# Kernel tuning notes

Measured on AMD Instinct MI355X. Metric: run time of the kernel, lower is better.

## Reference

```python
import jax, jax.numpy as jnp
import numpy as np

B, H, D = 4096, 200, 64
HID = 64


def setup_inputs() -> dict:
    key = jax.random.key(0)
    ks = jax.random.split(key, 12)
    s = 1.0 / np.sqrt(HID)
    return {
        "x": jax.random.normal(ks[0], (B, H, D), jnp.float32),
        "pos_query": jax.random.normal(ks[1], (B, D), jnp.float32),
        "lengths": jax.random.randint(ks[2], (B,), 1, H + 1, jnp.int32),
        "W_ih": jax.random.normal(ks[3], (3 * HID, D), jnp.float32) * s,
        "W_hh": jax.random.normal(ks[4], (3 * HID, HID), jnp.float32) * s,
        "b_ih": jax.random.normal(ks[5], (3 * HID,), jnp.float32) * s,
        "b_hh": jax.random.normal(ks[6], (3 * HID,), jnp.float32) * s,
        "aW_ih": jax.random.normal(ks[7], (3 * HID, HID), jnp.float32) * s,
        "aW_hh": jax.random.normal(ks[8], (3 * HID, HID), jnp.float32) * s,
        "ab_ih": jax.random.normal(ks[9], (3 * HID,), jnp.float32) * s,
        "ab_hh": jax.random.normal(ks[10], (3 * HID,), jnp.float32) * s,
    }


def _gates(x_t, h, W_i, W_h, b_i, b_h):
    gi = x_t @ W_i.T + b_i  # (B, 3H), PyTorch gate order [r, z, n]
    gh = h @ W_h.T + b_h
    gir, giz, gin = jnp.split(gi, 3, axis=-1)
    ghr, ghz, ghn = jnp.split(gh, 3, axis=-1)
    r = jax.nn.sigmoid(gir + ghr)
    z = jax.nn.sigmoid(giz + ghz)
    n = jnp.tanh(gin + r * ghn)
    return z, n


def _forward(x, pos_query, lengths, W_ih, W_hh, b_ih, b_hh, aW_ih, aW_hh, ab_ih, ab_hh):
    # mask[t, b] = True for valid (packed) timesteps
    mask = (jnp.arange(H)[:, None] < lengths[None, :])[:, :, None]  # (H, B, 1)
    xt = jnp.swapaxes(x, 0, 1)  # (H, B, D) time-major

    # --- GRU over packed sequence; padded positions output 0 (pad_packed_sequence) ---
    def gru_step(h, inp):
        x_t, m = inp
        z, n = _gates(x_t, h, W_ih, W_hh, b_ih, b_hh)
        h_new = (1.0 - z) * n + z * h
        h = jnp.where(m, h_new, h)
        return h, jnp.where(m, h_new, 0.0)

    h0 = jnp.zeros((x.shape[0], HID), x.dtype)
    _, out = jax.lax.scan(gru_step, h0, (xt, mask))  # out: (H, B, HID)

    # --- attention over full H (padded scores are 0, matching the torch code) ---
    scores = jnp.einsum("bd,hbd->bh", pos_query, out)  # (B, H)
    att = jax.nn.softmax(scores, axis=1)  # (B, H)

    # --- AUGRU: update gate scaled by attention score, masked to valid steps ---
    att_t = att.T[:, :, None]  # (H, B, 1)

    def augru_step(h, inp):
        o_t, a_t, m = inp
        u, n = _gates(o_t, h, aW_ih, aW_hh, ab_ih, ab_hh)
        u = a_t * u
        h_new = (1.0 - u) * h + u * n
        h = jnp.where(m, h_new, h)
        return h, None

    h_last, _ = jax.lax.scan(augru_step, h0, (out, att_t, mask))
    # h frozen past each sequence's length -> h_last == state at t = length-1
    return h_last  # (B, HID)


def reference(x, pos_query, lengths, W_ih, W_hh, b_ih, b_hh, aW_ih, aW_hh, ab_ih, ab_hh):
    return _forward(x, pos_query, lengths, W_ih, W_hh, b_ih, b_hh,
                    aW_ih, aW_hh, ab_ih, ab_hh)
```

## Files before the change

kernel.cpp:

```cpp
#include <hip/hip_runtime.h>
#include <hip/hip_bf16.h>


#define Bq   4096
#define Tq   200
#define BT   16

typedef __attribute__((ext_vector_type(8))) short short8;
typedef __attribute__((ext_vector_type(4))) float f32x4;

#define MFMA(a, b, c) __builtin_amdgcn_mfma_f32_16x16x32_bf16((a), (b), (c), 0, 0, 0)

#define LGKM_BARRIER()                                      \
  do {                                                      \
    __builtin_amdgcn_sched_barrier(0);                      \
    asm volatile("s_waitcnt lgkmcnt(0)" ::: "memory");      \
    __builtin_amdgcn_s_barrier();                           \
    asm volatile("" ::: "memory");                          \
    __builtin_amdgcn_sched_barrier(0);                      \
  } while (0)

static __device__ __forceinline__ int swz(int row, int colshort) {
  return row * 64 + ((((colshort) << 1) ^ ((row & 7) << 4)) >> 1);
}

static __device__ __forceinline__ unsigned pk2(float a, float b) {
  __hip_bfloat162 t = __float22bfloat162_rn(make_float2(a, b));
  unsigned r;
  __builtin_memcpy(&r, &t, sizeof(r));
  return r;
}
static __device__ __forceinline__ void pack4(f32x4 v, uint2 &H, uint2 &L) {
  H.x = pk2(v[0], v[1]);
  H.y = pk2(v[2], v[3]);
  float l0 = v[0] - __uint_as_float(H.x << 16);
  float l1 = v[1] - __uint_as_float(H.x & 0xffff0000u);
  float l2 = v[2] - __uint_as_float(H.y << 16);
  float l3 = v[3] - __uint_as_float(H.y & 0xffff0000u);
  L.x = pk2(l0, l1);
  L.y = pk2(l2, l3);
}
static __device__ __forceinline__ float sigm(float x) {
  return __builtin_amdgcn_rcpf(1.0f + __expf(-x));
}
static __device__ __forceinline__ float tanh_(float x) {
  return 2.0f * __builtin_amdgcn_rcpf(1.0f + __expf(-2.0f * x)) - 1.0f;
}
static __device__ __forceinline__ void split8(f32x4 a, f32x4 b, short8 &hi, short8 &lo) {
  uint2 H, L;
  pack4(a, H, L);
  hi[0] = (short)(H.x & 0xffff); hi[1] = (short)(H.x >> 16);
  hi[2] = (short)(H.y & 0xffff); hi[3] = (short)(H.y >> 16);
  lo[0] = (short)(L.x & 0xffff); lo[1] = (short)(L.x >> 16);
  lo[2] = (short)(L.y & 0xffff); lo[3] = (short)(L.y >> 16);
  pack4(b, H, L);
  hi[4] = (short)(H.x & 0xffff); hi[5] = (short)(H.x >> 16);
  hi[6] = (short)(H.y & 0xffff); hi[7] = (short)(H.y >> 16);
  lo[4] = (short)(L.x & 0xffff); lo[5] = (short)(L.x >> 16);
  lo[6] = (short)(L.y & 0xffff); lo[7] = (short)(L.y >> 16);
}

#define GI_X18(dR, dZ, dN, XH, XL)                   \
  _Pragma("unroll")                                  \
  for (int kc = 0; kc < 2; ++kc) {                   \
    dR = MFMA(wiH[0][kc], XH[kc], dR);               \
    dR = MFMA(wiH[0][kc], XL[kc], dR);               \
    dR = MFMA(wiL[0][kc], XH[kc], dR);               \
    dZ = MFMA(wiH[1][kc], XH[kc], dZ);               \
    dZ = MFMA(wiH[1][kc], XL[kc], dZ);               \
    dZ = MFMA(wiL[1][kc], XH[kc], dZ);               \
    dN = MFMA(wiH[2][kc], XH[kc], dN);               \
    dN = MFMA(wiH[2][kc], XL[kc], dN);               \
    dN = MFMA(wiL[2][kc], XH[kc], dN);               \
  }

#define GI_X12(dR, dZ, dN, XB)                       \
  _Pragma("unroll")                                  \
  for (int kc = 0; kc < 2; ++kc) {                   \
    dR = MFMA(wiH[0][kc], XB[kc], dR);               \
    dR = MFMA(wiL[0][kc], XB[kc], dR);               \
    dZ = MFMA(wiH[1][kc], XB[kc], dZ);               \
    dZ = MFMA(wiL[1][kc], XB[kc], dZ);               \
    dN = MFMA(wiH[2][kc], XB[kc], dN);               \
    dN = MFMA(wiL[2][kc], XB[kc], dN);               \
  }

#define GH18(dR, dZ, dNh)                            \
  _Pragma("unroll")                                  \
  for (int kc = 0; kc < 2; ++kc) {                   \
    dR  = MFMA(whH[0][kc], hH[kc], dR);              \
    dR  = MFMA(whH[0][kc], hL[kc], dR);              \
    dR  = MFMA(whL[0][kc], hH[kc], dR);              \
    dZ  = MFMA(whH[1][kc], hH[kc], dZ);              \
    dZ  = MFMA(whH[1][kc], hL[kc], dZ);              \
    dZ  = MFMA(whL[1][kc], hH[kc], dZ);              \
    dNh = MFMA(whH[2][kc], hH[kc], dNh);             \
    dNh = MFMA(whH[2][kc], hL[kc], dNh);             \
    dNh = MFMA(whL[2][kc], hH[kc], dNh);             \
  }

#define LOAD_WEIGHTS(WI, WH)                                                  \
  _Pragma("unroll")                                                           \
  for (int gt = 0; gt < 3; ++gt)                                              \
  _Pragma("unroll")                                                           \
    for (int kc = 0; kc < 2; ++kc) {                                          \
      const float* p = WI + (size_t)(gt * 64 + jh + c) * 64 + kc * 32 + g * 8;\
      split8(*(const f32x4*)p, *(const f32x4*)(p + 4), wiH[gt][kc], wiL[gt][kc]); \
      const float* q = WH + (size_t)(gt * 64 + jh + c) * 64 + kc * 32 + g * 8;\
      split8(*(const f32x4*)q, *(const f32x4*)(q + 4), whH[gt][kc], whL[gt][kc]); \
    }

#define LOAD_BIASES(BI, BH)                                                   \
  {                                                                           \
    f32x4 bi0 = *(const f32x4*)(BI + 0 * 64 + jh + 4 * g);                    \
    f32x4 bh0 = *(const f32x4*)(BH + 0 * 64 + jh + 4 * g);                    \
    f32x4 bi1 = *(const f32x4*)(BI + 1 * 64 + jh + 4 * g);                    \
    f32x4 bh1 = *(const f32x4*)(BH + 1 * 64 + jh + 4 * g);                    \
    bR = bi0 + bh0; bZ = bi1 + bh1;                                           \
    bNi = *(const f32x4*)(BI + 2 * 64 + jh + 4 * g);                          \
    bNh = *(const f32x4*)(BH + 2 * 64 + jh + 4 * g);                          \
  }

__global__ __launch_bounds__(256, 1)
void gru_fwd(const float* __restrict__ x, const float* __restrict__ pq,
             const int* __restrict__ lengths,
             const float* __restrict__ Wih, const float* __restrict__ Whh,
             const float* __restrict__ bih, const float* __restrict__ bhh,
             unsigned short* __restrict__ outbf,
             float* __restrict__ scores)
{
  __shared__ alignas(16) unsigned short hbH[2][1024], hbL[2][1024];
  __shared__ alignas(16) unsigned short xbH[2][1024], xbL[2][1024];
  __shared__ float slds[2][4][16];

  const int tid  = threadIdx.x;
  const int w    = tid >> 6;
  const int lane = tid & 63;
  const int c    = lane & 15;
  const int g    = lane >> 4;
  const int jh   = w * 16;
  const int b_g  = blockIdx.x * BT + c;

  const int pb   = tid >> 4;
  const int pd   = 4 * (tid & 15);
  const int pb_g = blockIdx.x * BT + pb;

  for (int i = tid; i < 1024; i += 256) { hbH[0][i] = 0; hbL[0][i] = 0; }

#pragma unroll
  for (int t0 = 0; t0 < 2; ++t0) {
    f32x4 xf = *(const f32x4*)(x + (size_t)pb_g * Tq * 64 + t0 * 64 + pd);
    uint2 H, L; pack4(xf, H, L);
    const int si = swz(pb, pd);
    *(uint2*)&xbH[t0][si] = H;
    *(uint2*)&xbL[t0][si] = L;
  }

  short8 wiH[3][2], wiL[3][2], whH[3][2], whL[3][2];
  LOAD_WEIGHTS(Wih, Whh);
  f32x4 bR, bZ, bNi, bNh;
  LOAD_BIASES(bih, bhh);
  const f32x4 pqv = *(const f32x4*)(pq + (size_t)b_g * 64 + jh + 4 * g);
  const int len = lengths[b_g];

  __syncthreads();

  f32x4 giR = bR, giZ = bZ, giN = bNi;
  {
    short8 xH[2], xL[2];
#pragma unroll
    for (int kc = 0; kc < 2; ++kc) {
      const int si = swz(c, kc * 32 + g * 8);
      xH[kc] = *(const short8*)&xbH[0][si];
      xL[kc] = *(const short8*)&xbL[0][si];
    }
    GI_X18(giR, giZ, giN, xH, xL);
  }

  f32x4 hreg = {0.f, 0.f, 0.f, 0.f};

  for (int t = 0; t < Tq; ++t) {
    const int cur = t & 1, nxt = cur ^ 1;
    const bool more = (t + 1 < Tq);

    f32x4 xf = {0.f, 0.f, 0.f, 0.f};
    if (t + 2 < Tq)
      xf = *(const f32x4*)(x + (size_t)pb_g * Tq * 64 + (size_t)(t + 2) * 64 + pd);

    short8 hH[2], hL[2], xnH[2], xnL[2];
#pragma unroll
    for (int kc = 0; kc < 2; ++kc) {
      const int si = swz(c, kc * 32 + g * 8);
      hH[kc] = *(const short8*)&hbH[cur][si];
      hL[kc] = *(const short8*)&hbL[cur][si];
    }
    if (more) {
#pragma unroll
      for (int kc = 0; kc < 2; ++kc) {
        const int si = swz(c, kc * 32 + g * 8);
        xnH[kc] = *(const short8*)&xbH[nxt][si];
        xnL[kc] = *(const short8*)&xbL[nxt][si];
      }
    }

    if (t > 0 && w == 0 && lane < 16) {
      float s = slds[nxt][0][lane] + slds[nxt][1][lane] +
                slds[nxt][2][lane] + slds[nxt][3][lane];
      scores[(size_t)(blockIdx.x * BT + lane) * Tq + (t - 1)] = s;
    }

    f32x4 aNh = bNh;
    GH18(giR, giZ, aNh);

    const bool valid = t < len;
    f32x4 outv;
#pragma unroll
    for (int r = 0; r < 4; ++r) {
      float rr = sigm(giR[r]);
      float zz = sigm(giZ[r]);
      float nn = tanh_(giN[r] + rr * aNh[r]);
      float hn = (1.f - zz) * nn + zz * hreg[r];
      hreg[r] = valid ? hn : hreg[r];
      outv[r] = valid ? hn : 0.f;
    }

    {
      uint2 H, L;
      pack4(hreg, H, L);
      const int si = swz(c, jh + 4 * g);
      *(uint2*)&hbH[nxt][si] = H;
      *(uint2*)&hbL[nxt][si] = L;
    }

    float sp = outv[0] * pqv[0] + outv[1] * pqv[1] + outv[2] * pqv[2] + outv[3] * pqv[3];
    sp += __shfl_xor(sp, 16);
    sp += __shfl_xor(sp, 32);
    if (lane < 16) slds[cur][w][lane] = sp;

    {
      uint2 O;
      O.x = pk2(outv[0], outv[1]);
      O.y = pk2(outv[2], outv[3]);
      *(uint2*)(outbf + (size_t)t * Bq * 64 + (size_t)b_g * 64 + jh + 4 * g) = O;
    }

    f32x4 nR = bR, nZ = bZ, nN = bNi;
    if (more) { GI_X18(nR, nZ, nN, xnH, xnL); }

    if (t + 2 < Tq) {
      uint2 H, L; pack4(xf, H, L);
      const int si = swz(pb, pd);
      *(uint2*)&xbH[cur][si] = H;
      *(uint2*)&xbL[cur][si] = L;
    }

    LGKM_BARRIER();
    giR = nR; giZ = nZ; giN = nN;
  }

  if (w == 0 && lane < 16) {
    const int pb2 = (Tq - 1) & 1;
    float s = slds[pb2][0][lane] + slds[pb2][1][lane] +
              slds[pb2][2][lane] + slds[pb2][3][lane];
    scores[(size_t)(blockIdx.x * BT + lane) * Tq + (Tq - 1)] = s;
  }
}

__global__ __launch_bounds__(256)
void softmax_att(const float* __restrict__ scores, float* __restrict__ att)
{
  const int w = threadIdx.x >> 6, lane = threadIdx.x & 63;
  const int row = blockIdx.x * 4 + w;
  const float* s = scores + (size_t)row * Tq;
  float v0 = s[lane], v1 = s[lane + 64], v2 = s[lane + 128];
  float v3 = (lane < Tq - 192) ? s[lane + 192] : -1e30f;
  float m = fmaxf(fmaxf(v0, v1), fmaxf(v2, v3));
#pragma unroll
  for (int off = 32; off >= 1; off >>= 1) m = fmaxf(m, __shfl_xor(m, off));
  float e0 = __expf(v0 - m), e1 = __expf(v1 - m), e2 = __expf(v2 - m);
  float e3 = (lane < Tq - 192) ? __expf(v3 - m) : 0.f;
  float sum = e0 + e1 + e2 + e3;
#pragma unroll
  for (int off = 32; off >= 1; off >>= 1) sum += __shfl_xor(sum, off);
  float inv = 1.f / sum;
  float* a = att + (size_t)row * Tq;
  a[lane] = e0 * inv;
  a[lane + 64] = e1 * inv;
  a[lane + 128] = e2 * inv;
  if (lane < Tq - 192) a[lane + 192] = e3 * inv;
}

__global__ __launch_bounds__(256, 1)
void augru_fwd(const unsigned short* __restrict__ outbf, const float* __restrict__ att,
               const int* __restrict__ lengths,
               const float* __restrict__ Wih, const float* __restrict__ Whh,
               const float* __restrict__ bih, const float* __restrict__ bhh,
               float* __restrict__ hout)
{
  __shared__ alignas(16) unsigned short hbH[2][1024], hbL[2][1024];
  __shared__ float att_lds[16][201];

  const int tid  = threadIdx.x;
  const int w    = tid >> 6;
  const int lane = tid & 63;
  const int c    = lane & 15;
  const int g    = lane >> 4;
  const int jh   = w * 16;
  const int b_g  = blockIdx.x * BT + c;

  for (int i = tid; i < 1024; i += 256) { hbH[0][i] = 0; hbL[0][i] = 0; }
  for (int i = tid; i < BT * Tq; i += 256)
    att_lds[i / Tq][i % Tq] = att[(size_t)blockIdx.x * BT * Tq + i];

  short8 wiH[3][2], wiL[3][2], whH[3][2], whL[3][2];
  LOAD_WEIGHTS(Wih, Whh);
  f32x4 bR, bZ, bNi, bNh;
  LOAD_BIASES(bih, bhh);
  const int len = lengths[b_g];

  f32x4 giR = bR, giZ = bZ, giN = bNi;
  {
    short8 x0[2];
#pragma unroll
    for (int kc = 0; kc < 2; ++kc)
      x0[kc] = *(const short8*)(outbf + (size_t)b_g * 64 + kc * 32 + g * 8);
    GI_X12(giR, giZ, giN, x0);
  }

  f32x4 hreg = {0.f, 0.f, 0.f, 0.f};
  __syncthreads();

  for (int t = 0; t < Tq; ++t) {
    const int cur = t & 1, nxt = cur ^ 1;
    const bool more = (t + 1 < Tq);

    short8 xn[2];
    if (more) {
#pragma unroll
      for (int kc = 0; kc < 2; ++kc)
        xn[kc] = *(const short8*)(outbf + (size_t)(t + 1) * Bq * 64 +
                                  (size_t)b_g * 64 + kc * 32 + g * 8);
    }

    short8 hH[2], hL[2];
#pragma unroll
    for (int kc = 0; kc < 2; ++kc) {
      const int si = swz(c, kc * 32 + g * 8);
      hH[kc] = *(const short8*)&hbH[cur][si];
      hL[kc] = *(const short8*)&hbL[cur][si];
    }
    const float a_t = att_lds[c][t];

    f32x4 aNh = bNh;
    GH18(giR, giZ, aNh);

    const bool valid = t < len;
#pragma unroll
    for (int r = 0; r < 4; ++r) {
      float rr = sigm(giR[r]);
      float uu = a_t * sigm(giZ[r]);
      float nn = tanh_(giN[r] + rr * aNh[r]);
      float hn = (1.f - uu) * hreg[r] + uu * nn;
      hreg[r] = valid ? hn : hreg[r];
    }

    {
      uint2 H, L;
      pack4(hreg, H, L);
      const int si = swz(c, jh + 4 * g);
      *(uint2*)&hbH[nxt][si] = H;
      *(uint2*)&hbL[nxt][si] = L;
    }

    f32x4 nR = bR, nZ = bZ, nN = bNi;
    if (more) { GI_X12(nR, nZ, nN, xn); }

    LGKM_BARRIER();
    giR = nR; giZ = nZ; giN = nN;
  }

  *(f32x4*)(hout + (size_t)b_g * 64 + jh + 4 * g) = hreg;
}

extern "C" void kernel_launch(void* const* d_in, const int* in_sizes, int n_in,
                              void* d_out, int out_size, void* d_ws, size_t ws_size,
                              hipStream_t stream)
{
  const float* x       = (const float*)d_in[0];
  const float* pq      = (const float*)d_in[1];
  const int*   lengths = (const int*)d_in[2];
  const float* Wih     = (const float*)d_in[3];
  const float* Whh     = (const float*)d_in[4];
  const float* bih     = (const float*)d_in[5];
  const float* bhh     = (const float*)d_in[6];
  const float* aWih    = (const float*)d_in[7];
  const float* aWhh    = (const float*)d_in[8];
  const float* abih    = (const float*)d_in[9];
  const float* abhh    = (const float*)d_in[10];
  float* hout = (float*)d_out;

  char* ws = (char*)d_ws;
  unsigned short* outbf = (unsigned short*)ws;
  float* scores = (float*)(ws + (size_t)Tq * Bq * 64 * 2);
  float* att    = scores + (size_t)Bq * Tq;

  gru_fwd<<<Bq / BT, 256, 0, stream>>>(x, pq, lengths, Wih, Whh, bih, bhh, outbf, scores);
  softmax_att<<<Bq / 4, 256, 0, stream>>>(scores, att);
  augru_fwd<<<Bq / BT, 256, 0, stream>>>(outbf, att, lengths, aWih, aWhh, abih, abhh, hout);
}
```

Measured before the change: 598.2 us.

## Warp-specialize GRU kernels: helper waves compute input gates via LDS

```diff
diff --git a/kernel.cpp b/kernel.cpp
--- a/kernel.cpp
+++ b/kernel.cpp
@@ -99,29 +99,7 @@
     dNh = MFMA(whL[2][kc], hH[kc], dNh);             \
   }
 
-#define LOAD_WEIGHTS(WI, WH)                                                  \
-  _Pragma("unroll")                                                           \
-  for (int gt = 0; gt < 3; ++gt)                                              \
-  _Pragma("unroll")                                                           \
-    for (int kc = 0; kc < 2; ++kc) {                                          \
-      const float* p = WI + (size_t)(gt * 64 + jh + c) * 64 + kc * 32 + g * 8;\
-      split8(*(const f32x4*)p, *(const f32x4*)(p + 4), wiH[gt][kc], wiL[gt][kc]); \
-      const float* q = WH + (size_t)(gt * 64 + jh + c) * 64 + kc * 32 + g * 8;\
-      split8(*(const f32x4*)q, *(const f32x4*)(q + 4), whH[gt][kc], whL[gt][kc]); \
-    }
-
-#define LOAD_BIASES(BI, BH)                                                   \
-  {                                                                           \
-    f32x4 bi0 = *(const f32x4*)(BI + 0 * 64 + jh + 4 * g);                    \
-    f32x4 bh0 = *(const f32x4*)(BH + 0 * 64 + jh + 4 * g);                    \
-    f32x4 bi1 = *(const f32x4*)(BI + 1 * 64 + jh + 4 * g);                    \
-    f32x4 bh1 = *(const f32x4*)(BH + 1 * 64 + jh + 4 * g);                    \
-    bR = bi0 + bh0; bZ = bi1 + bh1;                                           \
-    bNi = *(const f32x4*)(BI + 2 * 64 + jh + 4 * g);                          \
-    bNh = *(const f32x4*)(BH + 2 * 64 + jh + 4 * g);                          \
-  }
-
-__global__ __launch_bounds__(256, 1)
+__global__ __launch_bounds__(512, 1)
 void gru_fwd(const float* __restrict__ x, const float* __restrict__ pq,
              const int* __restrict__ lengths,
              const float* __restrict__ Wih, const float* __restrict__ Whh,
@@ -131,6 +109,7 @@
 {
   __shared__ alignas(16) unsigned short hbH[2][1024], hbL[2][1024];
   __shared__ alignas(16) unsigned short xbH[2][1024], xbL[2][1024];
+  __shared__ alignas(16) f32x4 gilds[2][3][256];
   __shared__ float slds[2][4][16];
 
   const int tid  = threadIdx.x;
@@ -138,35 +117,62 @@
   const int lane = tid & 63;
   const int c    = lane & 15;
   const int g    = lane >> 4;
-  const int jh   = w * 16;
+  const int jw   = w & 3;
+  const int jh   = jw * 16;
+  const bool helper = (w >= 4);
   const int b_g  = blockIdx.x * BT + c;
-
-  const int pb   = tid >> 4;
-  const int pd   = 4 * (tid & 15);
+  const int gl   = jw * 64 + lane;
+
+  const int hp   = tid & 255;
+  const int pb   = hp >> 4;
+  const int pd   = 4 * (hp & 15);
   const int pb_g = blockIdx.x * BT + pb;
 
-  for (int i = tid; i < 1024; i += 256) { hbH[0][i] = 0; hbL[0][i] = 0; }
-
-#pragma unroll
-  for (int t0 = 0; t0 < 2; ++t0) {
-    f32x4 xf = *(const f32x4*)(x + (size_t)pb_g * Tq * 64 + t0 * 64 + pd);
-    uint2 H, L; pack4(xf, H, L);
-    const int si = swz(pb, pd);
-    *(uint2*)&xbH[t0][si] = H;
-    *(uint2*)&xbL[t0][si] = L;
-  }
-
-  short8 wiH[3][2], wiL[3][2], whH[3][2], whL[3][2];
-  LOAD_WEIGHTS(Wih, Whh);
+  for (int i = tid; i < 1024; i += 512) { hbH[0][i] = 0; hbL[0][i] = 0; }
+
+  short8 wiH[3][2], wiL[3][2];
+  short8 whH[3][2], whL[3][2];
   f32x4 bR, bZ, bNi, bNh;
-  LOAD_BIASES(bih, bhh);
-  const f32x4 pqv = *(const f32x4*)(pq + (size_t)b_g * 64 + jh + 4 * g);
+  f32x4 pqv;
   const int len = lengths[b_g];
 
+  if (helper) {
+#pragma unroll
+    for (int t0 = 0; t0 < 2; ++t0) {
+      f32x4 xf = *(const f32x4*)(x + (size_t)pb_g * Tq * 64 + t0 * 64 + pd);
+      uint2 H, L; pack4(xf, H, L);
+      const int si = swz(pb, pd);
+      *(uint2*)&xbH[t0][si] = H;
+      *(uint2*)&xbL[t0][si] = L;
+    }
+#pragma unroll
+    for (int gt = 0; gt < 3; ++gt)
+#pragma unroll
+      for (int kc = 0; kc < 2; ++kc) {
+        const float* p = Wih + (size_t)(gt * 64 + jh + c) * 64 + kc * 32 + g * 8;
+        split8(*(const f32x4*)p, *(const f32x4*)(p + 4), wiH[gt][kc], wiL[gt][kc]);
+      }
+    f32x4 bi0 = *(const f32x4*)(bih + 0 * 64 + jh + 4 * g);
+    f32x4 bh0 = *(const f32x4*)(bhh + 0 * 64 + jh + 4 * g);
+    f32x4 bi1 = *(const f32x4*)(bih + 1 * 64 + jh + 4 * g);
+    f32x4 bh1 = *(const f32x4*)(bhh + 1 * 64 + jh + 4 * g);
+    bR = bi0 + bh0; bZ = bi1 + bh1;
+    bNi = *(const f32x4*)(bih + 2 * 64 + jh + 4 * g);
+  } else {
+#pragma unroll
+    for (int gt = 0; gt < 3; ++gt)
+#pragma unroll
+      for (int kc = 0; kc < 2; ++kc) {
+        const float* q = Whh + (size_t)(gt * 64 + jh + c) * 64 + kc * 32 + g * 8;
+        split8(*(const f32x4*)q, *(const f32x4*)(q + 4), whH[gt][kc], whL[gt][kc]);
+      }
+    bNh = *(const f32x4*)(bhh + 2 * 64 + jh + 4 * g);
+    pqv = *(const f32x4*)(pq + (size_t)b_g * 64 + jh + 4 * g);
+  }
+
   __syncthreads();
 
-  f32x4 giR = bR, giZ = bZ, giN = bNi;
-  {
+  if (helper) {
     short8 xH[2], xL[2];
 #pragma unroll
     for (int kc = 0; kc < 2; ++kc) {
@@ -174,91 +180,100 @@
       xH[kc] = *(const short8*)&xbH[0][si];
       xL[kc] = *(const short8*)&xbL[0][si];
     }
-    GI_X18(giR, giZ, giN, xH, xL);
-  }
-
+    f32x4 nR = bR, nZ = bZ, nN = bNi;
+    GI_X18(nR, nZ, nN, xH, xL);
+    gilds[0][0][gl] = nR;
+    gilds[0][1][gl] = nZ;
+    gilds[0][2][gl] = nN;
+  }
   f32x4 hreg = {0.f, 0.f, 0.f, 0.f};
+
+  __syncthreads();
 
   for (int t = 0; t < Tq; ++t) {
     const int cur = t & 1, nxt = cur ^ 1;
-    const bool more = (t + 1 < Tq);
-
-    f32x4 xf = {0.f, 0.f, 0.f, 0.f};
-    if (t + 2 < Tq)
-      xf = *(const f32x4*)(x + (size_t)pb_g * Tq * 64 + (size_t)(t + 2) * 64 + pd);
-
-    short8 hH[2], hL[2], xnH[2], xnL[2];
-#pragma unroll
-    for (int kc = 0; kc < 2; ++kc) {
-      const int si = swz(c, kc * 32 + g * 8);
-      hH[kc] = *(const short8*)&hbH[cur][si];
-      hL[kc] = *(const short8*)&hbL[cur][si];
-    }
-    if (more) {
+
+    if (!helper) {
+      short8 hH[2], hL[2];
 #pragma unroll
       for (int kc = 0; kc < 2; ++kc) {
         const int si = swz(c, kc * 32 + g * 8);
-        xnH[kc] = *(const short8*)&xbH[nxt][si];
-        xnL[kc] = *(const short8*)&xbL[nxt][si];
-      }
-    }
-
-    if (t > 0 && w == 0 && lane < 16) {
-      float s = slds[nxt][0][lane] + slds[nxt][1][lane] +
-                slds[nxt][2][lane] + slds[nxt][3][lane];
-      scores[(size_t)(blockIdx.x * BT + lane) * Tq + (t - 1)] = s;
-    }
-
-    f32x4 aNh = bNh;
-    GH18(giR, giZ, aNh);
-
-    const bool valid = t < len;
-    f32x4 outv;
-#pragma unroll
-    for (int r = 0; r < 4; ++r) {
-      float rr = sigm(giR[r]);
-      float zz = sigm(giZ[r]);
-      float nn = tanh_(giN[r] + rr * aNh[r]);
-      float hn = (1.f - zz) * nn + zz * hreg[r];
-      hreg[r] = valid ? hn : hreg[r];
-      outv[r] = valid ? hn : 0.f;
-    }
-
-    {
+        hH[kc] = *(const short8*)&hbH[cur][si];
+        hL[kc] = *(const short8*)&hbL[cur][si];
+      }
+      f32x4 aR  = gilds[cur][0][gl];
+      f32x4 aZ  = gilds[cur][1][gl];
+      f32x4 aNi = gilds[cur][2][gl];
+      f32x4 aNh = bNh;
+      GH18(aR, aZ, aNh);
+
+      const bool valid = t < len;
+      f32x4 outv;
+#pragma unroll
+      for (int r = 0; r < 4; ++r) {
+        float rr = sigm(aR[r]);
+        float zz = sigm(aZ[r]);
+        float nn = tanh_(aNi[r] + rr * aNh[r]);
+        float hn = (1.f - zz) * nn + zz * hreg[r];
+        hreg[r] = valid ? hn : hreg[r];
+        outv[r] = valid ? hn : 0.f;
+      }
+
       uint2 H, L;
       pack4(hreg, H, L);
-      const int si = swz(c, jh + 4 * g);
-      *(uint2*)&hbH[nxt][si] = H;
-      *(uint2*)&hbL[nxt][si] = L;
+      {
+        const int si = swz(c, jh + 4 * g);
+        *(uint2*)&hbH[nxt][si] = H;
+        *(uint2*)&hbL[nxt][si] = L;
+      }
+
+      float sp = outv[0] * pqv[0] + outv[1] * pqv[1] + outv[2] * pqv[2] + outv[3] * pqv[3];
+      sp += __shfl_xor(sp, 16);
+      sp += __shfl_xor(sp, 32);
+      if (lane < 16) slds[cur][jw][lane] = sp;
+
+      uint2 O;
+      O.x = valid ? H.x : 0u;
+      O.y = valid ? H.y : 0u;
+      *(uint2*)(outbf + (size_t)t * Bq * 64 + (size_t)b_g * 64 + jh + 4 * g) = O;
+    } else {
+      f32x4 xf = {0.f, 0.f, 0.f, 0.f};
+      if (t + 2 < Tq)
+        xf = *(const f32x4*)(x + (size_t)pb_g * Tq * 64 + (size_t)(t + 2) * 64 + pd);
+
+      if (t + 1 < Tq) {
+        short8 xH[2], xL[2];
+#pragma unroll
+        for (int kc = 0; kc < 2; ++kc) {
+          const int si = swz(c, kc * 32 + g * 8);
+          xH[kc] = *(const short8*)&xbH[nxt][si];
+          xL[kc] = *(const short8*)&xbL[nxt][si];
+        }
+        f32x4 nR = bR, nZ = bZ, nN = bNi;
+        GI_X18(nR, nZ, nN, xH, xL);
+        gilds[nxt][0][gl] = nR;
+        gilds[nxt][1][gl] = nZ;
+        gilds[nxt][2][gl] = nN;
+      }
+
+      if (t + 2 < Tq) {
+        uint2 H, L; pack4(xf, H, L);
+        const int si = swz(pb, pd);
+        *(uint2*)&xbH[cur][si] = H;
+        *(uint2*)&xbL[cur][si] = L;
+      }
+
+      if (t > 0 && w == 4 && lane < 16) {
+        float s = slds[nxt][0][lane] + slds[nxt][1][lane] +
+                  slds[nxt][2][lane] + slds[nxt][3][lane];
+        scores[(size_t)(blockIdx.x * BT + lane) * Tq + (t - 1)] = s;
+      }
     }
 
-    float sp = outv[0] * pqv[0] + outv[1] * pqv[1] + outv[2] * pqv[2] + outv[3] * pqv[3];
-    sp += __shfl_xor(sp, 16);
-    sp += __shfl_xor(sp, 32);
-    if (lane < 16) slds[cur][w][lane] = sp;
-
-    {
-      uint2 O;
-      O.x = pk2(outv[0], outv[1]);
-      O.y = pk2(outv[2], outv[3]);
-      *(uint2*)(outbf + (size_t)t * Bq * 64 + (size_t)b_g * 64 + jh + 4 * g) = O;
-    }
-
-    f32x4 nR = bR, nZ = bZ, nN = bNi;
-    if (more) { GI_X18(nR, nZ, nN, xnH, xnL); }
-
-    if (t + 2 < Tq) {
-      uint2 H, L; pack4(xf, H, L);
-      const int si = swz(pb, pd);
-      *(uint2*)&xbH[cur][si] = H;
-      *(uint2*)&xbL[cur][si] = L;
-    }
-
     LGKM_BARRIER();
-    giR = nR; giZ = nZ; giN = nN;
-  }
-
-  if (w == 0 && lane < 16) {
+  }
+
+  if (w == 4 && lane < 16) {
     const int pb2 = (Tq - 1) & 1;
     float s = slds[pb2][0][lane] + slds[pb2][1][lane] +
               slds[pb2][2][lane] + slds[pb2][3][lane];
@@ -290,7 +305,7 @@
   if (lane < Tq - 192) a[lane + 192] = e3 * inv;
 }
 
-__global__ __launch_bounds__(256, 1)
+__global__ __launch_bounds__(512, 1)
 void augru_fwd(const unsigned short* __restrict__ outbf, const float* __restrict__ att,
                const int* __restrict__ lengths,
                const float* __restrict__ Wih, const float* __restrict__ Whh,
@@ -298,6 +313,7 @@
                float* __restrict__ hout)
 {
   __shared__ alignas(16) unsigned short hbH[2][1024], hbL[2][1024];
+  __shared__ alignas(16) f32x4 gilds[2][3][256];
   __shared__ float att_lds[16][201];
 
   const int tid  = threadIdx.x;
@@ -305,81 +321,122 @@
   const int lane = tid & 63;
   const int c    = lane & 15;
   const int g    = lane >> 4;
-  const int jh   = w * 16;
+  const int jw   = w & 3;
+  const int jh   = jw * 16;
+  const bool helper = (w >= 4);
   const int b_g  = blockIdx.x * BT + c;
-
-  for (int i = tid; i < 1024; i += 256) { hbH[0][i] = 0; hbL[0][i] = 0; }
-  for (int i = tid; i < BT * Tq; i += 256)
+  const int gl   = jw * 64 + lane;
+
+  for (int i = tid; i < 1024; i += 512) { hbH[0][i] = 0; hbL[0][i] = 0; }
+  for (int i = tid; i < BT * Tq; i += 512)
     att_lds[i / Tq][i % Tq] = att[(size_t)blockIdx.x * BT * Tq + i];
 
-  short8 wiH[3][2], wiL[3][2], whH[3][2], whL[3][2];
-  LOAD_WEIGHTS(Wih, Whh);
+  short8 wiH[3][2], wiL[3][2];
+  short8 whH[3][2], whL[3][2];
   f32x4 bR, bZ, bNi, bNh;
-  LOAD_BIASES(bih, bhh);
   const int len = lengths[b_g];
 
-  f32x4 giR = bR, giZ = bZ, giN = bNi;
-  {
+  if (helper) {
+#pragma unroll
+    for (int gt = 0; gt < 3; ++gt)
+#pragma unroll
+      for (int kc = 0; kc < 2; ++kc) {
+        const float* p = Wih + (size_t)(gt * 64 + jh + c) * 64 + kc * 32 + g * 8;
+        split8(*(const f32x4*)p, *(const f32x4*)(p + 4), wiH[gt][kc], wiL[gt][kc]);
+      }
+    f32x4 bi0 = *(const f32x4*)(bih + 0 * 64 + jh + 4 * g);
+    f32x4 bh0 = *(const f32x4*)(bhh + 0 * 64 + jh + 4 * g);
+    f32x4 bi1 = *(const f32x4*)(bih + 1 * 64 + jh + 4 * g);
+    f32x4 bh1 = *(const f32x4*)(bhh + 1 * 64 + jh + 4 * g);
+    bR = bi0 + bh0; bZ = bi1 + bh1;
+    bNi = *(const f32x4*)(bih + 2 * 64 + jh + 4 * g);
+  } else {
+#pragma unroll
+    for (int gt = 0; gt < 3; ++gt)
+#pragma unroll
+      for (int kc = 0; kc < 2; ++kc) {
+        const float* q = Whh + (size_t)(gt * 64 + jh + c) * 64 + kc * 32 + g * 8;
+        split8(*(const f32x4*)q, *(const f32x4*)(q + 4), whH[gt][kc], whL[gt][kc]);
+      }
+    bNh = *(const f32x4*)(bhh + 2 * 64 + jh + 4 * g);
+  }
+
+  __syncthreads();
+
+  short8 xnA, xnB;
+  if (helper) {
     short8 x0[2];
 #pragma unroll
     for (int kc = 0; kc < 2; ++kc)
       x0[kc] = *(const short8*)(outbf + (size_t)b_g * 64 + kc * 32 + g * 8);
-    GI_X12(giR, giZ, giN, x0);
-  }
-
+    f32x4 nR = bR, nZ = bZ, nN = bNi;
+    GI_X12(nR, nZ, nN, x0);
+    gilds[0][0][gl] = nR;
+    gilds[0][1][gl] = nZ;
+    gilds[0][2][gl] = nN;
+    xnA = *(const short8*)(outbf + (size_t)1 * Bq * 64 + (size_t)b_g * 64 + 0 * 32 + g * 8);
+    xnB = *(const short8*)(outbf + (size_t)1 * Bq * 64 + (size_t)b_g * 64 + 1 * 32 + g * 8);
+  }
   f32x4 hreg = {0.f, 0.f, 0.f, 0.f};
+
   __syncthreads();
 
   for (int t = 0; t < Tq; ++t) {
     const int cur = t & 1, nxt = cur ^ 1;
-    const bool more = (t + 1 < Tq);
-
-    short8 xn[2];
-    if (more) {
-#pragma unroll
-      for (int kc = 0; kc < 2; ++kc)
-        xn[kc] = *(const short8*)(outbf + (size_t)(t + 1) * Bq * 64 +
-                                  (size_t)b_g * 64 + kc * 32 + g * 8);
-    }
-
-    short8 hH[2], hL[2];
-#pragma unroll
-    for (int kc = 0; kc < 2; ++kc) {
-      const int si = swz(c, kc * 32 + g * 8);
-      hH[kc] = *(const short8*)&hbH[cur][si];
-      hL[kc] = *(const short8*)&hbL[cur][si];
-    }
-    const float a_t = att_lds[c][t];
-
-    f32x4 aNh = bNh;
-    GH18(giR, giZ, aNh);
-
-    const bool valid = t < len;
-#pragma unroll
-    for (int r = 0; r < 4; ++r) {
-      float rr = sigm(giR[r]);
-      float uu = a_t * sigm(giZ[r]);
-      float nn = tanh_(giN[r] + rr * aNh[r]);
-      float hn = (1.f - uu) * hreg[r] + uu * nn;
-      hreg[r] = valid ? hn : hreg[r];
-    }
-
-    {
+
+    if (!helper) {
+      short8 hH[2], hL[2];
+#pragma unroll
+      for (int kc = 0; kc < 2; ++kc) {
+        const int si = swz(c, kc * 32 + g * 8);
+        hH[kc] = *(const short8*)&hbH[cur][si];
+        hL[kc] = *(const short8*)&hbL[cur][si];
+      }
+      f32x4 aR  = gilds[cur][0][gl];
+      f32x4 aZ  = gilds[cur][1][gl];
+      f32x4 aNi = gilds[cur][2][gl];
+      f32x4 aNh = bNh;
+      GH18(aR, aZ, aNh);
+
+      const float a_t = att_lds[c][t];
+      const bool valid = t < len;
+#pragma unroll
+      for (int r = 0; r < 4; ++r) {
+        float rr = sigm(aR[r]);
+        float uu = a_t * sigm(aZ[r]);
+        float nn = tanh_(aNi[r] + rr * aNh[r]);
+        float hn = (1.f - uu) * hreg[r] + uu * nn;
+        hreg[r] = valid ? hn : hreg[r];
+      }
+
       uint2 H, L;
       pack4(hreg, H, L);
       const int si = swz(c, jh + 4 * g);
       *(uint2*)&hbH[nxt][si] = H;
       *(uint2*)&hbL[nxt][si] = L;
+    } else {
+      if (t + 1 < Tq) {
+        short8 xb2[2];
+        xb2[0] = xnA; xb2[1] = xnB;
+        f32x4 nR = bR, nZ = bZ, nN = bNi;
+        GI_X12(nR, nZ, nN, xb2);
+        gilds[nxt][0][gl] = nR;
+        gilds[nxt][1][gl] = nZ;
+        gilds[nxt][2][gl] = nN;
+      }
+      if (t + 2 < Tq) {
+        xnA = *(const short8*)(outbf + (size_t)(t + 2) * Bq * 64 +
+                               (size_t)b_g * 64 + 0 * 32 + g * 8);
+        xnB = *(const short8*)(outbf + (size_t)(t + 2) * Bq * 64 +
+                               (size_t)b_g * 64 + 1 * 32 + g * 8);
+      }
     }
 
-    f32x4 nR = bR, nZ = bZ, nN = bNi;
-    if (more) { GI_X12(nR, nZ, nN, xn); }
-
     LGKM_BARRIER();
-    giR = nR; giZ = nZ; giN = nN;
-  }
-
-  *(f32x4*)(hout + (size_t)b_g * 64 + jh + 4 * g) = hreg;
+  }
+
+  if (!helper)
+    *(f32x4*)(hout + (size_t)b_g * 64 + jh + 4 * g) = hreg;
 }
 
 extern "C" void kernel_launch(void* const* d_in, const int* in_sizes, int n_in,
@@ -404,7 +461,7 @@
   float* scores = (float*)(ws + (size_t)Tq * Bq * 64 * 2);
   float* att    = scores + (size_t)Bq * Tq;
 
-  gru_fwd<<<Bq / BT, 256, 0, stream>>>(x, pq, lengths, Wih, Whh, bih, bhh, outbf, scores);
+  gru_fwd<<<Bq / BT, 512, 0, stream>>>(x, pq, lengths, Wih, Whh, bih, bhh, outbf, scores);
   softmax_att<<<Bq / 4, 256, 0, stream>>>(scores, att);
-  augru_fwd<<<Bq / BT, 256, 0, stream>>>(outbf, att, lengths, aWih, aWhh, abih, abhh, hout);
-}
+  augru_fwd<<<Bq / BT, 512, 0, stream>>>(outbf, att, lengths, aWih, aWhh, abih, abhh, hout);
+}
```

Measured after the change: 583.4 us. -2.5%, faster.
